# Kernel tuning notes

Hardware: AMD Instinct MI355X
Metric: run time of the kernel (lower is better)

Reference implementation:

```python
import jax, jax.numpy as jnp
import numpy as np

N = 50000
E = 625000
D_IN, D_HID, D_OUT = 128, 128, 64


def setup_inputs() -> dict:
    key = jax.random.key(0)
    k1, k2, k3, k4 = jax.random.split(key, 4)
    x = jax.random.normal(k1, (N, D_IN), dtype=jnp.float32)
    edge_index = jax.random.randint(k2, (2, E), 0, N, dtype=jnp.int32)
    # Glorot-ish init for linear weights (PyG lin has no bias; bias added after agg)
    W1 = jax.random.normal(k3, (D_HID, D_IN), dtype=jnp.float32) / np.sqrt(D_IN)
    b1 = jnp.zeros((D_HID,), dtype=jnp.float32)
    W2 = jax.random.normal(k4, (D_OUT, D_HID), dtype=jnp.float32) / np.sqrt(D_HID)
    b2 = jnp.zeros((D_OUT,), dtype=jnp.float32)
    return {"x": x, "edge_index": edge_index, "W1": W1, "b1": b1, "W2": W2, "b2": b2}


def _gcn_conv(x, W, b, src, dst, n):
    # GCNConv: h = x @ W^T; out[dst] += norm * h[src]; out += b
    # src/dst already include self-loops; symmetric normalization deg^{-1/2}.
    ones = jnp.ones(src.shape[0], dtype=x.dtype)
    deg = jax.ops.segment_sum(ones, dst, num_segments=n)
    dinv = jnp.where(deg > 0, jax.lax.rsqrt(deg), 0.0)
    norm = dinv[src] * dinv[dst]                      # [E+N]
    h = x @ W.T                                        # [N, d_out]
    msg = norm[:, None] * h[src]                       # [E+N, d_out]
    out = jax.ops.segment_sum(msg, dst, num_segments=n)
    return out + b


def reference(x, edge_index, W1, b1, W2, b2):
    n = x.shape[0]
    loops = jnp.arange(n, dtype=edge_index.dtype)
    src = jnp.concatenate([edge_index[0], loops])      # add self-loops
    dst = jnp.concatenate([edge_index[1], loops])
    h = _gcn_conv(x, W1, b1, src, dst, n)
    h = jax.nn.relu(h)
    out = _gcn_conv(h, W2, b2, src, dst, n)
    return out
```

## Files before the change

### kernel.cpp

```cpp
#include <hip/hip_runtime.h>
#include <hip/hip_bf16.h>


typedef __attribute__((ext_vector_type(8))) __bf16 bf16x8;
typedef __attribute__((ext_vector_type(8))) unsigned short ushort8;
typedef __attribute__((ext_vector_type(4))) float floatx4;

static __device__ __forceinline__ float bf2f(unsigned short s) {
    unsigned u = ((unsigned)s) << 16;
    return __builtin_bit_cast(float, u);
}
static __device__ __forceinline__ unsigned short f2bf(float f) {
    unsigned u = __builtin_bit_cast(unsigned, f);
    unsigned r = (u + 0x7FFFu + ((u >> 16) & 1u)) >> 16;
    return (unsigned short)r;
}
static __device__ __forceinline__ void ld8f(const void* p, size_t idx, int isbf, float* o) {
    if (isbf) {
        ushort8 t = __builtin_bit_cast(ushort8, *(const int4*)((const unsigned short*)p + idx));
        #pragma unroll
        for (int j = 0; j < 8; ++j) o[j] = bf2f(t[j]);
    } else {
        const float* f = (const float*)p + idx;
        float4 a = *(const float4*)f;
        float4 b = *(const float4*)(f + 4);
        o[0]=a.x; o[1]=a.y; o[2]=a.z; o[3]=a.w; o[4]=b.x; o[5]=b.y; o[6]=b.z; o[7]=b.w;
    }
}
static __device__ __forceinline__ int4 ld8frag(const void* p, size_t idx, int isbf) {
    if (isbf) {
        return *(const int4*)((const unsigned short*)p + idx);
    } else {
        const float* f = (const float*)p + idx;
        float4 a = *(const float4*)f;
        float4 b = *(const float4*)(f + 4);
        ushort8 t;
        t[0]=f2bf(a.x); t[1]=f2bf(a.y); t[2]=f2bf(a.z); t[3]=f2bf(a.w);
        t[4]=f2bf(b.x); t[5]=f2bf(b.y); t[6]=f2bf(b.z); t[7]=f2bf(b.w);
        return __builtin_bit_cast(int4, t);
    }
}
static __device__ __forceinline__ float bread(const void* p, int i, int isbf) {
    return isbf ? bf2f(((const unsigned short*)p)[i]) : ((const float*)p)[i];
}

__global__ __launch_bounds__(256) void k_countdet(
    const int* __restrict__ src, const int* __restrict__ dst,
    int* __restrict__ cnt, int E, int EB, int qdiv,
    const unsigned* __restrict__ xw, int* __restrict__ flag)
{
    int b = blockIdx.x;
    if (b == EB) {
        __shared__ int red[256];
        int t = threadIdx.x;
        int c = 0;
        #pragma unroll
        for (int i = 0; i < 16; ++i) {
            unsigned w = xw[t * 16 + i];
            unsigned exp = (w >> 7) & 0xFFu;
            c += (exp <= 0x84u) ? 1 : 0;
        }
        red[t] = c;
        __syncthreads();
        for (int s = 128; s > 0; s >>= 1) {
            if (t < s) red[t] += red[t + s];
            __syncthreads();
        }
        if (t == 0) flag[0] = (red[0] >= 3686) ? 1 : 0;
        return;
    }
    int e = b * 256 + threadIdx.x;
    if (e < E) {
        int s = src[e], d = dst[e];
        int q = s / qdiv; q = (q > 3) ? 3 : q;
        atomicAdd(&cnt[d * 4 + q], 1);
    }
}

__global__ __launch_bounds__(256) void k_scanA(
    const int* __restrict__ cnt, int* __restrict__ partial, int M)
{
    int b = blockIdx.x, t = threadIdx.x;
    int base = b * 1024 + t * 4;
    int s = 0;
    if (base + 3 < M) {
        int4 v = *(const int4*)&cnt[base];
        s = v.x + v.y + v.z + v.w;
    } else {
        for (int j = 0; j < 4; ++j) { int i = base + j; if (i < M) s += cnt[i]; }
    }
    #pragma unroll
    for (int d = 1; d < 64; d <<= 1) s += __shfl_down(s, d, 64);
    __shared__ int ws[4];
    int lane = t & 63, wid = t >> 6;
    if (lane == 0) ws[wid] = s;
    __syncthreads();
    if (t == 0) partial[b] = ws[0] + ws[1] + ws[2] + ws[3];
}

__global__ __launch_bounds__(256) void k_scanC(
    const int* __restrict__ cnt, const int* __restrict__ partial,
    int* __restrict__ off, int* __restrict__ cursor, float* __restrict__ dinv,
    int M, int nb)
{
    __shared__ int s_pref, s_tot;
    int b = blockIdx.x, t = threadIdx.x, lane = t & 63, wid = t >> 6;
    if (t == 0) {
        int s = 0, pb = 0;
        for (int i = 0; i < nb; ++i) { if (i == b) pb = s; s += partial[i]; }
        s_pref = pb; s_tot = s;
    }
    int base = b * 1024 + t * 4;
    int v[4], s = 0;
    #pragma unroll
    for (int j = 0; j < 4; ++j) {
        int i = base + j;
        v[j] = (i < M) ? cnt[i] : 0;
        s += v[j];
    }
    int x = s;
    #pragma unroll
    for (int d = 1; d < 64; d <<= 1) {
        int u = __shfl_up(x, d, 64);
        if (lane >= d) x += u;
    }
    __shared__ int wtot[4], woff[4];
    if (lane == 63) wtot[wid] = x;
    __syncthreads();
    if (t == 0) {
        int a = 0;
        #pragma unroll
        for (int w = 0; w < 4; ++w) { woff[w] = a; a += wtot[w]; }
    }
    __syncthreads();
    int excl = s_pref + woff[wid] + (x - s);
    #pragma unroll
    for (int j = 0; j < 4; ++j) {
        int i = base + j;
        if (i < M) {
            off[i] = excl;
            cursor[i] = excl;
            excl += v[j];
        }
    }
    if (base < M) {
        int node = base >> 2;
        dinv[node] = rsqrtf(1.0f + (float)s);
    }
    if (b == 0 && t == 0) off[M] = s_tot;
}

__global__ void k_scatter(const int* __restrict__ src, const int* __restrict__ dst,
                          const float* __restrict__ dinv,
                          int* __restrict__ cursor, int2* __restrict__ bucket,
                          int E, int qdiv) {
    int e = blockIdx.x * 256 + threadIdx.x;
    if (e >= E) return;
    int s = src[e], d = dst[e];
    int q = s / qdiv; q = (q > 3) ? 3 : q;
    float w = dinv[s] * dinv[d];
    int pos = atomicAdd(&cursor[d * 4 + q], 1);
    int2 rec; rec.x = s; rec.y = __builtin_bit_cast(int, w);
    bucket[pos] = rec;
}

__global__ __launch_bounds__(256) void k_gather1(
    const void* __restrict__ x, const float* __restrict__ dinv,
    const int* __restrict__ off, const int2* __restrict__ bucket,
    unsigned short* __restrict__ z1, int N, const int* __restrict__ flag)
{
    int isbf = *flag;
    int gid = blockIdx.x * 256 + threadIdx.x;
    int node = gid >> 4, p = gid & 15;
    if (node >= N) return;
    float di = dinv[node];
    float acc[8], va[8], vb[8];
    ld8f(x, (size_t)node * 128 + p * 8, isbf, va);
    float w0 = di * di;
    #pragma unroll
    for (int j = 0; j < 8; ++j) acc[j] = w0 * va[j];
    int it = off[node * 4], s1 = off[node * 4 + 4];
    for (; it + 1 < s1; it += 2) {
        int2 ea = bucket[it], eb = bucket[it + 1];
        float wa = __builtin_bit_cast(float, ea.y);
        float wb = __builtin_bit_cast(float, eb.y);
        ld8f(x, (size_t)ea.x * 128 + p * 8, isbf, va);
        ld8f(x, (size_t)eb.x * 128 + p * 8, isbf, vb);
        #pragma unroll
        for (int j = 0; j < 8; ++j) acc[j] += wa * va[j] + wb * vb[j];
    }
    if (it < s1) {
        int2 ea = bucket[it];
        float wa = __builtin_bit_cast(float, ea.y);
        ld8f(x, (size_t)ea.x * 128 + p * 8, isbf, va);
        #pragma unroll
        for (int j = 0; j < 8; ++j) acc[j] += wa * va[j];
    }
    ushort8 o;
    #pragma unroll
    for (int j = 0; j < 8; ++j) o[j] = f2bf(acc[j]);
    *(int4*)&z1[(size_t)node * 128 + p * 8] = __builtin_bit_cast(int4, o);
}

__global__ __launch_bounds__(256) void k_gemm12(
    const unsigned short* __restrict__ z1, const void* __restrict__ W1,
    const void* __restrict__ b1, const void* __restrict__ W2,
    unsigned short* __restrict__ h2, int N, const int* __restrict__ flag)
{
    int isbf = *flag;
    __shared__ int4 w1f[2048];
    __shared__ unsigned short h1t[4][16 * 136];
    int tid = threadIdx.x;
    for (int u = tid; u < 2048; u += 256) {
        int nt = u >> 8, kt = (u >> 6) & 3, lane = u & 63;
        int so = (nt * 16 + (lane & 15)) * 128 + kt * 32 + ((lane >> 4) << 3);
        w1f[u] = ld8frag(W1, so, isbf);
    }
    int wave = tid >> 6, lane = tid & 63, m = lane & 15, quad = lane >> 4;

    int4 w2r[4][4];
    #pragma unroll
    for (int nt = 0; nt < 4; ++nt)
        #pragma unroll
        for (int kt = 0; kt < 4; ++kt)
            w2r[nt][kt] = ld8frag(W2, (nt * 16 + m) * 128 + kt * 32 + quad * 8, isbf);
    __syncthreads();

    int ntile = (N + 15) >> 4;
    int tile = blockIdx.x * 4 + wave;
    int tcl = (tile < ntile) ? tile : (ntile - 1);
    int arow = tcl * 16 + m;
    if (arow >= N) arow = N - 1;

    bf16x8 a[4];
    #pragma unroll
    for (int kt = 0; kt < 4; ++kt)
        a[kt] = __builtin_bit_cast(bf16x8, *(const int4*)&z1[(size_t)arow * 128 + kt * 32 + quad * 8]);
    floatx4 acc[8];
    floatx4 z = {0.f, 0.f, 0.f, 0.f};
    #pragma unroll
    for (int nt = 0; nt < 8; ++nt) acc[nt] = z;
    #pragma unroll
    for (int kt = 0; kt < 4; ++kt)
        #pragma unroll
        for (int nt = 0; nt < 8; ++nt) {
            bf16x8 b = __builtin_bit_cast(bf16x8, w1f[nt * 256 + kt * 64 + lane]);
            acc[nt] = __builtin_amdgcn_mfma_f32_16x16x32_bf16(a[kt], b, acc[nt], 0, 0, 0);
        }
    #pragma unroll
    for (int nt = 0; nt < 8; ++nt) {
        int col = nt * 16 + m;
        float bb = bread(b1, col, isbf);
        #pragma unroll
        for (int r = 0; r < 4; ++r) {
            float v = acc[nt][r] + bb;
            h1t[wave][(quad * 4 + r) * 136 + col] = f2bf(fmaxf(v, 0.f));
        }
    }
    __syncthreads();

    bf16x8 a2[4];
    #pragma unroll
    for (int kt = 0; kt < 4; ++kt)
        a2[kt] = __builtin_bit_cast(bf16x8, *(const int4*)&h1t[wave][m * 136 + kt * 32 + quad * 8]);
    floatx4 acc2[4];
    #pragma unroll
    for (int nt = 0; nt < 4; ++nt) acc2[nt] = z;
    #pragma unroll
    for (int kt = 0; kt < 4; ++kt)
        #pragma unroll
        for (int nt = 0; nt < 4; ++nt) {
            bf16x8 b = __builtin_bit_cast(bf16x8, w2r[nt][kt]);
            acc2[nt] = __builtin_amdgcn_mfma_f32_16x16x32_bf16(a2[kt], b, acc2[nt], 0, 0, 0);
        }
    if (tile < ntile) {
        int rbase = tcl * 16 + quad * 4;
        #pragma unroll
        for (int nt = 0; nt < 4; ++nt) {
            int col = nt * 16 + m;
            #pragma unroll
            for (int r = 0; r < 4; ++r) {
                int orow = rbase + r;
                if (orow < N)
                    h2[(size_t)orow * 64 + col] = f2bf(acc2[nt][r]);
            }
        }
    }
}

__global__ __launch_bounds__(256) void k_gather2(
    const unsigned short* __restrict__ h2, const float* __restrict__ dinv,
    const int* __restrict__ off, const int2* __restrict__ bucket,
    const void* __restrict__ b2, void* __restrict__ out, int N,
    const int* __restrict__ flag)
{
    int isbf = *flag;
    int gid = blockIdx.x * 256 + threadIdx.x;
    int node = gid >> 3, p = gid & 7;
    if (node >= N) return;
    float di = dinv[node];
    float acc[8];
    {
        ushort8 t = __builtin_bit_cast(ushort8, *(const int4*)&h2[(size_t)node * 64 + p * 8]);
        float w0 = di * di;
        #pragma unroll
        for (int j = 0; j < 8; ++j) acc[j] = w0 * bf2f(t[j]);
    }
    int it = off[node * 4], s1 = off[node * 4 + 4];
    for (; it + 1 < s1; it += 2) {
        int2 ea = bucket[it], eb = bucket[it + 1];
        float wa = __builtin_bit_cast(float, ea.y);
        float wb = __builtin_bit_cast(float, eb.y);
        ushort8 ta = __builtin_bit_cast(ushort8, *(const int4*)&h2[(size_t)ea.x * 64 + p * 8]);
        ushort8 tb = __builtin_bit_cast(ushort8, *(const int4*)&h2[(size_t)eb.x * 64 + p * 8]);
        #pragma unroll
        for (int j = 0; j < 8; ++j) acc[j] += wa * bf2f(ta[j]) + wb * bf2f(tb[j]);
    }
    if (it < s1) {
        int2 ea = bucket[it];
        float wa = __builtin_bit_cast(float, ea.y);
        ushort8 ta = __builtin_bit_cast(ushort8, *(const int4*)&h2[(size_t)ea.x * 64 + p * 8]);
        #pragma unroll
        for (int j = 0; j < 8; ++j) acc[j] += wa * bf2f(ta[j]);
    }
    #pragma unroll
    for (int j = 0; j < 8; ++j) acc[j] += bread(b2, p * 8 + j, isbf);
    if (isbf) {
        ushort8 o;
        #pragma unroll
        for (int j = 0; j < 8; ++j) o[j] = f2bf(acc[j]);
        *(int4*)((unsigned short*)out + (size_t)node * 64 + p * 8) = __builtin_bit_cast(int4, o);
    } else {
        float* fo = (float*)out + (size_t)node * 64 + p * 8;
        float4 a = {acc[0], acc[1], acc[2], acc[3]};
        float4 b = {acc[4], acc[5], acc[6], acc[7]};
        *(float4*)fo = a;
        *(float4*)(fo + 4) = b;
    }
}

extern "C" void kernel_launch(void* const* d_in, const int* in_sizes, int n_in,
                              void* d_out, int out_size, void* d_ws, size_t ws_size,
                              hipStream_t stream) {
    const void* x  = d_in[0];
    const int*  ei = (const int*)d_in[1];
    const void* W1 = d_in[2];
    const void* b1 = d_in[3];
    const void* W2 = d_in[4];
    const void* b2 = d_in[5];

    int N = in_sizes[0] / 128;
    int E = in_sizes[1] / 2;
    const int* srcI = ei;
    const int* dstI = ei + E;

    int M = N * 4;
    int qdiv = (N + 3) / 4;
    int nb = (M + 1023) / 1024;
    int EB = (E + 255) / 256;

    char* base = (char*)d_ws;
    size_t o = 0;
    auto take = [&](size_t bytes) { size_t r = o; o += (bytes + 255) & ~(size_t)255; return r; };
    int*   flag    = (int*)  (base + take(4));
    int*   cnt     = (int*)  (base + take((size_t)M * 4));
    int*   off     = (int*)  (base + take((size_t)(M + 1) * 4));
    int*   cursor  = (int*)  (base + take((size_t)M * 4));
    float* dinv    = (float*)(base + take((size_t)N * 4));
    int*   partial = (int*)  (base + take((size_t)nb * 4));
    int2*  bucket  = (int2*) (base + take((size_t)E * 8));
    unsigned short* z1 = (unsigned short*)(base + take((size_t)N * 128 * 2));
    unsigned short* h2 = (unsigned short*)(base + take((size_t)N * 64 * 2));

    int ntile = (N + 15) / 16;
    int gemmBlocks = (ntile + 3) / 4;

    hipMemsetAsync(cnt, 0, (size_t)M * 4, stream);
    k_countdet<<<EB + 1, 256, 0, stream>>>(srcI, dstI, cnt, E, EB, qdiv, (const unsigned*)x, flag);
    k_scanA<<<nb, 256, 0, stream>>>(cnt, partial, M);
    k_scanC<<<nb, 256, 0, stream>>>(cnt, partial, off, cursor, dinv, M, nb);
    k_scatter<<<EB, 256, 0, stream>>>(srcI, dstI, dinv, cursor, bucket, E, qdiv);
    k_gather1<<<(N * 16 + 255) / 256, 256, 0, stream>>>(x, dinv, off, bucket, z1, N, flag);
    k_gemm12<<<gemmBlocks, 256, 0, stream>>>(z1, W1, b1, W2, h2, N, flag);
    k_gather2<<<(N * 8 + 255) / 256, 256, 0, stream>>>(h2, dinv, off, bucket, b2, d_out, N, flag);
}
```

Before: 244.4 us.

## Bin edges into 16 fixed source ranges per destination and unroll layer-1 gather

Edges for each destination are now bucketed by source-node range `src >> 12`, giving 16 segments of 4096 nodes instead of 4 quarters. Concurrent gathers therefore touch a narrower, more cache-resident slice of the feature matrix. The degree normalisation moves into a separate `k_dinv` kernel that reads the offsets, the count array is reused in place as the scatter cursor, and the layer-1 gather loop is unrolled by four to keep more loads in flight. In exchange the count/offset arrays grow fourfold, and the serial per-block partial-sum loop in the scan covers four times as many blocks, which adds prefix-sum overhead.

```diff
diff --git a/kernel.cpp b/kernel.cpp
--- a/kernel.cpp
+++ b/kernel.cpp
@@ -5,6 +5,9 @@
 typedef __attribute__((ext_vector_type(8))) __bf16 bf16x8;
 typedef __attribute__((ext_vector_type(8))) unsigned short ushort8;
 typedef __attribute__((ext_vector_type(4))) float floatx4;
+
+#define SEG 16
+#define QSH 12
 
 static __device__ __forceinline__ float bf2f(unsigned short s) {
     unsigned u = ((unsigned)s) << 16;
@@ -46,7 +49,7 @@
 
 __global__ __launch_bounds__(256) void k_countdet(
     const int* __restrict__ src, const int* __restrict__ dst,
-    int* __restrict__ cnt, int E, int EB, int qdiv,
+    int* __restrict__ cnt, int E, int EB,
     const unsigned* __restrict__ xw, int* __restrict__ flag)
 {
     int b = blockIdx.x;
@@ -72,8 +75,8 @@
     int e = b * 256 + threadIdx.x;
     if (e < E) {
         int s = src[e], d = dst[e];
-        int q = s / qdiv; q = (q > 3) ? 3 : q;
-        atomicAdd(&cnt[d * 4 + q], 1);
+        int q = s >> QSH; q = (q > SEG - 1) ? (SEG - 1) : q;
+        atomicAdd(&cnt[d * SEG + q], 1);
     }
 }
 
@@ -100,8 +103,7 @@
 
 __global__ __launch_bounds__(256) void k_scanC(
     const int* __restrict__ cnt, const int* __restrict__ partial,
-    int* __restrict__ off, int* __restrict__ cursor, float* __restrict__ dinv,
-    int M, int nb)
+    int* __restrict__ off, int* __restrict__ cursor, int M, int nb)
 {
     __shared__ int s_pref, s_tot;
     int b = blockIdx.x, t = threadIdx.x, lane = t & 63, wid = t >> 6;
@@ -143,23 +145,26 @@
             excl += v[j];
         }
     }
-    if (base < M) {
-        int node = base >> 2;
-        dinv[node] = rsqrtf(1.0f + (float)s);
-    }
     if (b == 0 && t == 0) off[M] = s_tot;
+}
+
+__global__ void k_dinv(const int* __restrict__ off, float* __restrict__ dinv, int N) {
+    int i = blockIdx.x * 256 + threadIdx.x;
+    if (i < N) {
+        int deg = off[(i + 1) * SEG] - off[i * SEG];
+        dinv[i] = rsqrtf(1.0f + (float)deg);
+    }
 }
 
 __global__ void k_scatter(const int* __restrict__ src, const int* __restrict__ dst,
                           const float* __restrict__ dinv,
-                          int* __restrict__ cursor, int2* __restrict__ bucket,
-                          int E, int qdiv) {
+                          int* __restrict__ cursor, int2* __restrict__ bucket, int E) {
     int e = blockIdx.x * 256 + threadIdx.x;
     if (e >= E) return;
     int s = src[e], d = dst[e];
-    int q = s / qdiv; q = (q > 3) ? 3 : q;
+    int q = s >> QSH; q = (q > SEG - 1) ? (SEG - 1) : q;
     float w = dinv[s] * dinv[d];
-    int pos = atomicAdd(&cursor[d * 4 + q], 1);
+    int pos = atomicAdd(&cursor[d * SEG + q], 1);
     int2 rec; rec.x = s; rec.y = __builtin_bit_cast(int, w);
     bucket[pos] = rec;
 }
@@ -174,22 +179,27 @@
     int node = gid >> 4, p = gid & 15;
     if (node >= N) return;
     float di = dinv[node];
-    float acc[8], va[8], vb[8];
+    float acc[8], va[8], vb[8], vc[8], vd[8];
     ld8f(x, (size_t)node * 128 + p * 8, isbf, va);
     float w0 = di * di;
     #pragma unroll
     for (int j = 0; j < 8; ++j) acc[j] = w0 * va[j];
-    int it = off[node * 4], s1 = off[node * 4 + 4];
-    for (; it + 1 < s1; it += 2) {
-        int2 ea = bucket[it], eb = bucket[it + 1];
+    int it = off[node * SEG], s1 = off[node * SEG + SEG];
+    for (; it + 3 < s1; it += 4) {
+        int2 ea = bucket[it], eb = bucket[it + 1], ec = bucket[it + 2], ed = bucket[it + 3];
         float wa = __builtin_bit_cast(float, ea.y);
         float wb = __builtin_bit_cast(float, eb.y);
+        float wc = __builtin_bit_cast(float, ec.y);
+        float wd = __builtin_bit_cast(float, ed.y);
         ld8f(x, (size_t)ea.x * 128 + p * 8, isbf, va);
         ld8f(x, (size_t)eb.x * 128 + p * 8, isbf, vb);
-        #pragma unroll
-        for (int j = 0; j < 8; ++j) acc[j] += wa * va[j] + wb * vb[j];
-    }
-    if (it < s1) {
+        ld8f(x, (size_t)ec.x * 128 + p * 8, isbf, vc);
+        ld8f(x, (size_t)ed.x * 128 + p * 8, isbf, vd);
+        #pragma unroll
+        for (int j = 0; j < 8; ++j)
+            acc[j] += wa * va[j] + wb * vb[j] + wc * vc[j] + wd * vd[j];
+    }
+    for (; it < s1; ++it) {
         int2 ea = bucket[it];
         float wa = __builtin_bit_cast(float, ea.y);
         ld8f(x, (size_t)ea.x * 128 + p * 8, isbf, va);
@@ -306,7 +316,7 @@
         #pragma unroll
         for (int j = 0; j < 8; ++j) acc[j] = w0 * bf2f(t[j]);
     }
-    int it = off[node * 4], s1 = off[node * 4 + 4];
+    int it = off[node * SEG], s1 = off[node * SEG + SEG];
     for (; it + 1 < s1; it += 2) {
         int2 ea = bucket[it], eb = bucket[it + 1];
         float wa = __builtin_bit_cast(float, ea.y);
@@ -354,8 +364,7 @@
     const int* srcI = ei;
     const int* dstI = ei + E;
 
-    int M = N * 4;
-    int qdiv = (N + 3) / 4;
+    int M = N * SEG;
     int nb = (M + 1023) / 1024;
     int EB = (E + 255) / 256;
 
@@ -365,21 +374,22 @@
     int*   flag    = (int*)  (base + take(4));
     int*   cnt     = (int*)  (base + take((size_t)M * 4));
     int*   off     = (int*)  (base + take((size_t)(M + 1) * 4));
-    int*   cursor  = (int*)  (base + take((size_t)M * 4));
     float* dinv    = (float*)(base + take((size_t)N * 4));
     int*   partial = (int*)  (base + take((size_t)nb * 4));
     int2*  bucket  = (int2*) (base + take((size_t)E * 8));
     unsigned short* z1 = (unsigned short*)(base + take((size_t)N * 128 * 2));
     unsigned short* h2 = (unsigned short*)(base + take((size_t)N * 64 * 2));
+    int* cursor = cnt;
 
     int ntile = (N + 15) / 16;
     int gemmBlocks = (ntile + 3) / 4;
 
     hipMemsetAsync(cnt, 0, (size_t)M * 4, stream);
-    k_countdet<<<EB + 1, 256, 0, stream>>>(srcI, dstI, cnt, E, EB, qdiv, (const unsigned*)x, flag);
+    k_countdet<<<EB + 1, 256, 0, stream>>>(srcI, dstI, cnt, E, EB, (const unsigned*)x, flag);
     k_scanA<<<nb, 256, 0, stream>>>(cnt, partial, M);
-    k_scanC<<<nb, 256, 0, stream>>>(cnt, partial, off, cursor, dinv, M, nb);
-    k_scatter<<<EB, 256, 0, stream>>>(srcI, dstI, dinv, cursor, bucket, E, qdiv);
+    k_scanC<<<nb, 256, 0, stream>>>(cnt, partial, off, cursor, M, nb);
+    k_dinv<<<(N + 255) / 256, 256, 0, stream>>>(off, dinv, N);
+    k_scatter<<<EB, 256, 0, stream>>>(srcI, dstI, dinv, cursor, bucket, E);
     k_gather1<<<(N * 16 + 255) / 256, 256, 0, stream>>>(x, dinv, off, bucket, z1, N, flag);
     k_gemm12<<<gemmBlocks, 256, 0, stream>>>(z1, W1, b1, W2, h2, N, flag);
     k_gather2<<<(N * 8 + 255) / 256, 256, 0, stream>>>(h2, dinv, off, bucket, b2, d_out, N, flag);
```

Measured after the change: 278.7 us. +14.0%, slower.
